# Kernel tuning notes

Measured on AMD Instinct MI355X. Metric: run time of the kernel, lower is better.

## Reference

```python
import jax, jax.numpy as jnp
import numpy as np

K = 2
BN_EPS = 1e-5


def setup_inputs() -> dict:
    key = jax.random.key(0)
    k1, k2, k3 = jax.random.split(key, 3)
    B, C, H, W, D, O = 4, 128, 32, 32, 32, 128
    x = jax.random.normal(k1, (B, C, H, W, D), dtype=jnp.float32)
    conv_w = jax.random.normal(k2, (O, 2 * C), dtype=jnp.float32) * 0.02  # 1x1x1 conv kernel
    conv_b = jax.random.normal(k3, (O,), dtype=jnp.float32) * 0.02
    bn_gamma = jnp.ones((O,), dtype=jnp.float32)
    bn_beta = jnp.zeros((O,), dtype=jnp.float32)
    return {"x": x, "conv_w": conv_w, "conv_b": conv_b,
            "bn_gamma": bn_gamma, "bn_beta": bn_beta}


def _axis_running_max(x, x_j, axis, dim):
    # torch.cat([x[..., -i:], x[..., :-i]], axis) == jnp.roll(x, i, axis)
    shifts = jnp.arange(K, dim, K)

    def step(carry, s):
        diff = x - jnp.roll(x, s, axis=axis)
        return jnp.maximum(carry, diff), None

    x_j, _ = jax.lax.scan(step, x_j, shifts)
    return x_j


def reference(x, conv_w, conv_b, bn_gamma, bn_beta):
    B, C, H, W, D = x.shape
    x_j = jnp.zeros_like(x)
    x_j = _axis_running_max(x, x_j, 2, H)
    x_j = _axis_running_max(x, x_j, 3, W)
    x_j = _axis_running_max(x, x_j, 4, D)
    x_j = jax.lax.stop_gradient(x_j)  # original detaches every x_j update

    xc = jnp.concatenate([x, x_j], axis=1)  # [B, 2C, H, W, D]
    # 1x1x1 Conv3d == per-voxel channel GEMM
    y = jnp.einsum('bchwd,oc->bohwd', xc, conv_w) + conv_b[None, :, None, None, None]

    # BatchNorm3d, training mode (batch statistics over B,H,W,D)
    mean = y.mean(axis=(0, 2, 3, 4), keepdims=True)
    var = ((y - mean) ** 2).mean(axis=(0, 2, 3, 4), keepdims=True)
    yn = (y - mean) * jax.lax.rsqrt(var + BN_EPS)
    yn = yn * bn_gamma[None, :, None, None, None] + bn_beta[None, :, None, None, None]

    # torch nn.GELU default is exact erf form
    return jax.nn.gelu(yn, approximate=False)
```

## Files before the change

### kernel.cpp

```cpp
#include <hip/hip_runtime.h>
#include <hip/hip_bf16.h>

#define BB 4
#define CCH 128
#define C2 256
#define OO 128
#define NVOX 32768
#define NTOT (BB*NVOX)
#define NGB 1024

typedef __attribute__((ext_vector_type(4))) float f32x4;
typedef __attribute__((ext_vector_type(8))) short s16x8;
typedef __attribute__((ext_vector_type(4))) unsigned int u32x4;
typedef __attribute__((ext_vector_type(2))) unsigned int u32x2;
typedef unsigned int u32;
typedef unsigned short u16;

#define SWZ(r) ((((r)>>3) ^ (r)) & 7)

__device__ __forceinline__ float bf2f(short s){
  union { u32 i; float f; } cv; cv.i = ((u32)(u16)s) << 16; return cv.f;
}
__device__ __forceinline__ short f2bf(float f){
  union { __hip_bfloat16 h; short s; } cv; cv.h = __float2bfloat16(f); return cv.s;
}
__device__ __forceinline__ u32 pack2(float a, float b){
  return ((u32)(u16)f2bf(a)) | (((u32)(u16)f2bf(b)) << 16);
}
__device__ __forceinline__ float ulo(u32 r){
  union { u32 i; float f; } cv; cv.i = r << 16; return cv.f;
}
__device__ __forceinline__ float uhi(u32 r){
  union { u32 i; float f; } cv; cv.i = r & 0xffff0000u; return cv.f;
}

__global__ __launch_bounds__(256) void k_convw(const float* __restrict__ w, short* __restrict__ wb){
  int i = blockIdx.x*256 + threadIdx.x;
  wb[i] = f2bf(w[i]);
}


__device__ __forceinline__ int swz3(int h, int w, int bin){
  int s1 = ((w>>1) ^ h) & 3;
  int s2 = ((w>>3) ^ (h>>2)) & 3;
  return (h<<11) + ((w ^ s2)<<6) + ((bin & 15) | (((((bin>>4)) ^ s1) & 3) << 4));
}

__global__ __launch_bounds__(512, 4) void k_xj(const float* __restrict__ x, short* __restrict__ xc){
  __shared__ __align__(16) u32 xs[16384];
  __shared__ __align__(16) u32 tw[2048];
  __shared__ __align__(16) u32 th[2048];
  int t = threadIdx.x;
  u32 bc = blockIdx.x;
  const float* __restrict__ src = x + (size_t)bc*NVOX;

  #pragma unroll
  for(int j=0;j<16;j++){
    int e0 = (t + 512*j)*4;
    f32x4 v = *(const f32x4*)(src + e0);
    int h = e0>>10, w = (e0>>5)&31, bin = (e0&31)*2;
    u32* dst = (u32*)((char*)xs + swz3(h,w,bin));
    dst[0] = pack2(v[0], v[1]);
    dst[1] = pack2(v[2], v[3]);
  }
  __syncthreads();

  {
    int dq = t & 7, aa = (t >> 3) & 31;
    float m1[2][4], m2[2][4];
    #pragma unroll
    for(int p=0;p<2;p++)
      #pragma unroll
      for(int k=0;k<4;k++){ m1[p][k]=1e30f; m2[p][k]=1e30f; }
    if(t < 256){
      int h = aa;
      #pragma unroll
      for(int w=0;w<32;w++){
        int p = w & 1;
        u32x2 g = *(const u32x2*)((const char*)xs + swz3(h,w,dq*8));
        #pragma unroll
        for(int q=0;q<2;q++){
          float a = ulo(g[q]), b = uhi(g[q]);
          m2[p][2*q]   = fminf(m2[p][2*q],   fmaxf(m1[p][2*q],   a)); m1[p][2*q]   = fminf(m1[p][2*q],   a);
          m2[p][2*q+1] = fminf(m2[p][2*q+1], fmaxf(m1[p][2*q+1], b)); m1[p][2*q+1] = fminf(m1[p][2*q+1], b);
        }
      }
      #pragma unroll
      for(int p=0;p<2;p++){
        u32 o0 = pack2(m1[p][0], m2[p][0]), o1 = pack2(m1[p][1], m2[p][1]);
        u32 o2 = pack2(m1[p][2], m2[p][2]), o3 = pack2(m1[p][3], m2[p][3]);
        *(u32x4*)&tw[h*64 + p*32 + dq*4] = (u32x4){o0,o1,o2,o3};
      }
    } else {
      int w = aa;
      #pragma unroll
      for(int h=0;h<32;h++){
        int p = h & 1;
        u32x2 g = *(const u32x2*)((const char*)xs + swz3(h,w,dq*8));
        #pragma unroll
        for(int q=0;q<2;q++){
          float a = ulo(g[q]), b = uhi(g[q]);
          m2[p][2*q]   = fminf(m2[p][2*q],   fmaxf(m1[p][2*q],   a)); m1[p][2*q]   = fminf(m1[p][2*q],   a);
          m2[p][2*q+1] = fminf(m2[p][2*q+1], fmaxf(m1[p][2*q+1], b)); m1[p][2*q+1] = fminf(m1[p][2*q+1], b);
        }
      }
      #pragma unroll
      for(int p=0;p<2;p++){
        u32 o0 = pack2(m1[p][0], m2[p][0]), o1 = pack2(m1[p][1], m2[p][1]);
        u32 o2 = pack2(m1[p][2], m2[p][2]), o3 = pack2(m1[p][3], m2[p][3]);
        *(u32x4*)&th[p*1024 + w*32 + ((dq ^ (w&7))*4)] = (u32x4){o0,o1,o2,o3};
      }
    }
  }
  __syncthreads();

  short* __restrict__ px = xc + ((size_t)((bc>>7)*C2 + (bc&127)))*NVOX;
  short* __restrict__ pj = px + (size_t)CCH*NVOX;
  #pragma unroll
  for(int j=0;j<2;j++){
    int l = t + 512*j;
    int h = l>>5, w = l&31;
    u32x4 xr[4];
    #pragma unroll
    for(int g=0;g<4;g++)
      xr[g] = *(const u32x4*)((const char*)xs + swz3(h,w,g<<4));
    float xv[32];
    #pragma unroll
    for(int g=0;g<4;g++)
      #pragma unroll
      for(int q=0;q<4;q++){
        xv[g*8+2*q]   = ulo(xr[g][q]);
        xv[g*8+2*q+1] = uhi(xr[g][q]);
      }
    float m1d[2] = {1e30f,1e30f}, m2d[2] = {1e30f,1e30f};
    #pragma unroll
    for(int q=0;q<16;q++){
      m2d[0] = fminf(m2d[0], fmaxf(m1d[0], xv[2*q]));   m1d[0] = fminf(m1d[0], xv[2*q]);
      m2d[1] = fminf(m2d[1], fmaxf(m1d[1], xv[2*q+1])); m1d[1] = fminf(m1d[1], xv[2*q+1]);
    }
    const u32* twr = &tw[h*64 + (w&1)*32];
    int thbase = (h&1)*1024 + w*32, ws7 = w&7;
    u32 xjp[16];
    #pragma unroll
    for(int q=0;q<8;q++){
      u32x4 wv = *(const u32x4*)(twr + q*4);
      u32x4 hv = *(const u32x4*)(&th[thbase + ((q ^ ws7)*4)]);
      float o4[4];
      #pragma unroll
      for(int i=0;i<4;i++){
        int d = q*4 + i, p = d & 1;
        float xvv = xv[d];
        float meD = (xvv == m1d[p]) ? m2d[p] : m1d[p];
        float w1 = ulo(wv[i]);
        float meW = (xvv == w1) ? uhi(wv[i]) : w1;
        float h1 = ulo(hv[i]);
        float meH = (xvv == h1) ? uhi(hv[i]) : h1;
        float m = fminf(meD, fminf(meW, meH));
        o4[i] = fmaxf(0.0f, xvv - m);
      }
      xjp[q*2]   = pack2(o4[0], o4[1]);
      xjp[q*2+1] = pack2(o4[2], o4[3]);
    }
    #pragma unroll
    for(int g=0;g<4;g++){
      *(u32x4*)(px + (size_t)l*32 + g*8) = xr[g];
      *(u32x4*)(pj + (size_t)l*32 + g*8) = (u32x4){xjp[g*4],xjp[g*4+1],xjp[g*4+2],xjp[g*4+3]};
    }
  }
}

__global__ __launch_bounds__(256) void k_gemm(const short* __restrict__ xc, const short* __restrict__ wb,
                                              short* __restrict__ y, float* __restrict__ part){
  __shared__ __align__(16) char lds[32768];
  u32 blk = blockIdx.x;
  u32 vblk = blk & 255, b = blk >> 8;
  u32 vbase = vblk * 128;
  const short* __restrict__ xb = xc + (size_t)b*C2*NVOX + vbase;
  int t = threadIdx.x;
  int wave = t >> 6, lane = t & 63;
  int wr = wave >> 1, wc = wave & 1;
  int l15 = lane & 15, l4 = lane >> 4;
  f32x4 acc[4][4];
  #pragma unroll
  for(int mt=0;mt<4;mt++)
    #pragma unroll
    for(int nt=0;nt<4;nt++) acc[mt][nt] = (f32x4){0.f,0.f,0.f,0.f};

  int v0  = (t & 15) * 8;
  int cb2 = 2 * (t >> 4);

  #pragma unroll
  for(int kc=0;kc<2;kc++){
    s16x8 ra[4], rb[4];
    #pragma unroll
    for(int q=0;q<4;q++){
      const short* src = xb + (size_t)(kc*128 + cb2 + 32*q)*NVOX + v0;
      ra[q] = *(const s16x8*)(src);
      rb[q] = *(const s16x8*)(src + NVOX);
    }
    __syncthreads();
    #pragma unroll
    for(int q=0;q<4;q++){
      int c = cb2 + 32*q;
      #pragma unroll
      for(int e=0;e<8;e++){
        int v = v0 + e;
        u32 pr = ((u32)(u16)ra[q][e]) | (((u32)(u16)rb[q][e]) << 16);
        *(u32*)(lds + v*256 + ((((c>>3) ^ SWZ(v))<<4) | ((c&7)<<1))) = pr;
      }
    }
    __syncthreads();
    #pragma unroll
    for(int ks=0;ks<4;ks++){
      int kk = ks*32 + l4*8;
      s16x8 afrag[4], bfrag[4];
      #pragma unroll
      for(int nt=0;nt<4;nt++){
        int vloc = wc*64 + nt*16 + l15;
        bfrag[nt] = *(const s16x8*)(lds + vloc*256 + (((kk>>3) ^ SWZ(vloc))<<4));
      }
      #pragma unroll
      for(int mt=0;mt<4;mt++){
        int o = wr*64 + mt*16 + l15;
        afrag[mt] = *(const s16x8*)(wb + o*C2 + kc*128 + kk);
      }
      #pragma unroll
      for(int mt=0;mt<4;mt++)
        #pragma unroll
        for(int nt=0;nt<4;nt++)
          acc[mt][nt] = __builtin_amdgcn_mfma_f32_16x16x32_bf16(afrag[mt], bfrag[nt], acc[mt][nt], 0,0,0);
    }
  }

  __syncthreads();
  #pragma unroll
  for(int mt=0;mt<4;mt++){
    #pragma unroll
    for(int nt=0;nt<4;nt++){
      int vcol = wc*64 + nt*16 + l15;
      #pragma unroll
      for(int r=0;r<4;r++){
        int o = wr*64 + mt*16 + l4*4 + r;
        *(short*)(lds + o*256 + ((((vcol>>3) ^ SWZ(o))<<4) | ((vcol&7)<<1))) = f2bf(acc[mt][nt][r]);
      }
    }
  }
  __syncthreads();
  short* __restrict__ yb = y + (size_t)b*OO*NVOX + vbase;
  #pragma unroll
  for(int q=0;q<8;q++){
    int p = t + q*256;
    int o = p >> 4, vs = (p & 15) * 8;
    s16x8 val = *(const s16x8*)(lds + o*256 + ((((vs>>3) ^ SWZ(o))<<4)));
    *(s16x8*)(yb + (size_t)o*NVOX + vs) = val;
  }

  {
    int o = t >> 1, vh = t & 1;
    float sm = 0.f, ss = 0.f;
    #pragma unroll
    for(int k=0;k<8;k++){
      int vs = vh*64 + k*8;
      s16x8 val = *(const s16x8*)(lds + o*256 + ((((vs>>3) ^ SWZ(o))<<4)));
      #pragma unroll
      for(int e=0;e<8;e++){ float f = bf2f(val[e]); sm += f; ss += f*f; }
    }
    sm += __shfl_xor(sm, 1);
    ss += __shfl_xor(ss, 1);
    if(vh == 0){
      float* pp = part + ((size_t)blk*OO + o)*2;
      pp[0] = sm; pp[1] = ss;
    }
  }
}

__global__ __launch_bounds__(256) void k_statsf(const float* __restrict__ part, float* __restrict__ stats){
  int o = blockIdx.x, t = threadIdx.x;
  float sm = 0.f, ss = 0.f;
  #pragma unroll
  for(int k=0;k<4;k++){
    int blk = t + k*256;
    const float* pp = part + ((size_t)blk*OO + o)*2;
    sm += pp[0]; ss += pp[1];
  }
  __shared__ float rs[256], rss[256];
  rs[t] = sm; rss[t] = ss;
  __syncthreads();
  for(int k=128;k>0;k>>=1){
    if(t<k){ rs[t]+=rs[t+k]; rss[t]+=rss[t+k]; }
    __syncthreads();
  }
  if(t==0){
    float inv = 1.0f/(float)NTOT;
    float mean = rs[0]*inv;
    float var = rss[0]*inv - mean*mean;
    stats[2*o]   = mean;
    stats[2*o+1] = rsqrtf(var + 1e-5f);
  }
}

__global__ __launch_bounds__(256) void k_bngelu(const short* __restrict__ y, const float* __restrict__ stats,
                                                const float* __restrict__ gamma, const float* __restrict__ beta,
                                                float* __restrict__ out){
  size_t base = ((size_t)blockIdx.x*256 + threadIdx.x)*8;
  int o = (int)((base >> 15) & 127);
  float mean = stats[2*o], rstd = stats[2*o+1];
  float g  = gamma[o]*rstd;
  float be = beta[o] - mean*g;
  s16x8 u = *(const s16x8*)(y + base);
  f32x4 r0, r1;
  #pragma unroll
  for(int e=0;e<8;e++){
    float yn = bf2f(u[e])*g + be;
    float ge = 0.5f*yn*(1.0f + erff(yn*0.70710678118654752f));
    if(e<4) r0[e] = ge; else r1[e-4] = ge;
  }
  *(f32x4*)(out + base)     = r0;
  *(f32x4*)(out + base + 4) = r1;
}

extern "C" void kernel_launch(void* const* d_in, const int* in_sizes, int n_in,
                              void* d_out, int out_size, void* d_ws, size_t ws_size,
                              hipStream_t stream) {
  (void)in_sizes; (void)n_in; (void)out_size; (void)ws_size;
  const float* x     = (const float*)d_in[0];
  const float* cw    = (const float*)d_in[1];
  const float* gamma = (const float*)d_in[3];
  const float* beta  = (const float*)d_in[4];
  float* out = (float*)d_out;

  char* ws = (char*)d_ws;
  short* wb    = (short*)ws;
  short* y     = (short*)(ws + 65536);
  float* stats = (float*)(ws + 65536 + (size_t)BB*OO*NVOX*2);
  float* part  = stats + 256;
  short* xcbuf = (short*)d_out;

  k_convw <<<dim3((OO*C2)/256),     dim3(256), 0, stream>>>(cw, wb);
  k_xj    <<<dim3(BB*CCH),         dim3(512), 0, stream>>>(x, xcbuf);
  k_gemm  <<<dim3(BB*(NVOX/128)),  dim3(256), 0, stream>>>(xcbuf, wb, y, part);
  k_statsf<<<dim3(OO),             dim3(256), 0, stream>>>(part, stats);
  k_bngelu<<<dim3((NTOT*OO)/2048), dim3(256), 0, stream>>>(y, stats, gamma, beta, out);
}
```

Measured before the change: 98.80 us.

## Drop LDS staging of x slab in prep kernel; read axis minima from global

The prep kernel no longer stages the full 32x32x32 bf16 slab in a 64KB shared buffer. The W and H axis two-smallest reductions now read x directly from global memory, with each thread handling one (h,d) or (w,d) line. The per-row D pass reloads its row from global. This frees most of the shared memory so more blocks can be resident per CU. In exchange each x element is read from global about three times, relying on cache hits, and the strided W/H reads are scalar loads.

```diff
diff --git a/kernel.cpp b/kernel.cpp
--- a/kernel.cpp
+++ b/kernel.cpp
@@ -7,12 +7,10 @@
 #define OO 128
 #define NVOX 32768
 #define NTOT (BB*NVOX)
-#define NGB 1024
 
 typedef __attribute__((ext_vector_type(4))) float f32x4;
 typedef __attribute__((ext_vector_type(8))) short s16x8;
 typedef __attribute__((ext_vector_type(4))) unsigned int u32x4;
-typedef __attribute__((ext_vector_type(2))) unsigned int u32x2;
 typedef unsigned int u32;
 typedef unsigned short u16;
 
@@ -33,21 +31,14 @@
 __device__ __forceinline__ float uhi(u32 r){
   union { u32 i; float f; } cv; cv.i = r & 0xffff0000u; return cv.f;
 }
+__device__ __forceinline__ float bfr(float f){ return bf2f(f2bf(f)); }
 
 __global__ __launch_bounds__(256) void k_convw(const float* __restrict__ w, short* __restrict__ wb){
   int i = blockIdx.x*256 + threadIdx.x;
   wb[i] = f2bf(w[i]);
 }
 
-
-__device__ __forceinline__ int swz3(int h, int w, int bin){
-  int s1 = ((w>>1) ^ h) & 3;
-  int s2 = ((w>>3) ^ (h>>2)) & 3;
-  return (h<<11) + ((w ^ s2)<<6) + ((bin & 15) | (((((bin>>4)) ^ s1) & 3) << 4));
-}
-
-__global__ __launch_bounds__(512, 4) void k_xj(const float* __restrict__ x, short* __restrict__ xc){
-  __shared__ __align__(16) u32 xs[16384];
+__global__ __launch_bounds__(512) void k_prep(const float* __restrict__ x, short* __restrict__ xc){
   __shared__ __align__(16) u32 tw[2048];
   __shared__ __align__(16) u32 th[2048];
   int t = threadIdx.x;
@@ -55,62 +46,33 @@
   const float* __restrict__ src = x + (size_t)bc*NVOX;
 
   #pragma unroll
-  for(int j=0;j<16;j++){
-    int e0 = (t + 512*j)*4;
-    f32x4 v = *(const f32x4*)(src + e0);
-    int h = e0>>10, w = (e0>>5)&31, bin = (e0&31)*2;
-    u32* dst = (u32*)((char*)xs + swz3(h,w,bin));
-    dst[0] = pack2(v[0], v[1]);
-    dst[1] = pack2(v[2], v[3]);
-  }
-  __syncthreads();
-
-  {
-    int dq = t & 7, aa = (t >> 3) & 31;
-    float m1[2][4], m2[2][4];
-    #pragma unroll
-    for(int p=0;p<2;p++)
-      #pragma unroll
-      for(int k=0;k<4;k++){ m1[p][k]=1e30f; m2[p][k]=1e30f; }
-    if(t < 256){
-      int h = aa;
-      #pragma unroll
-      for(int w=0;w<32;w++){
-        int p = w & 1;
-        u32x2 g = *(const u32x2*)((const char*)xs + swz3(h,w,dq*8));
-        #pragma unroll
-        for(int q=0;q<2;q++){
-          float a = ulo(g[q]), b = uhi(g[q]);
-          m2[p][2*q]   = fminf(m2[p][2*q],   fmaxf(m1[p][2*q],   a)); m1[p][2*q]   = fminf(m1[p][2*q],   a);
-          m2[p][2*q+1] = fminf(m2[p][2*q+1], fmaxf(m1[p][2*q+1], b)); m1[p][2*q+1] = fminf(m1[p][2*q+1], b);
-        }
-      }
-      #pragma unroll
-      for(int p=0;p<2;p++){
-        u32 o0 = pack2(m1[p][0], m2[p][0]), o1 = pack2(m1[p][1], m2[p][1]);
-        u32 o2 = pack2(m1[p][2], m2[p][2]), o3 = pack2(m1[p][3], m2[p][3]);
-        *(u32x4*)&tw[h*64 + p*32 + dq*4] = (u32x4){o0,o1,o2,o3};
-      }
-    } else {
-      int w = aa;
-      #pragma unroll
-      for(int h=0;h<32;h++){
-        int p = h & 1;
-        u32x2 g = *(const u32x2*)((const char*)xs + swz3(h,w,dq*8));
-        #pragma unroll
-        for(int q=0;q<2;q++){
-          float a = ulo(g[q]), b = uhi(g[q]);
-          m2[p][2*q]   = fminf(m2[p][2*q],   fmaxf(m1[p][2*q],   a)); m1[p][2*q]   = fminf(m1[p][2*q],   a);
-          m2[p][2*q+1] = fminf(m2[p][2*q+1], fmaxf(m1[p][2*q+1], b)); m1[p][2*q+1] = fminf(m1[p][2*q+1], b);
-        }
-      }
-      #pragma unroll
-      for(int p=0;p<2;p++){
-        u32 o0 = pack2(m1[p][0], m2[p][0]), o1 = pack2(m1[p][1], m2[p][1]);
-        u32 o2 = pack2(m1[p][2], m2[p][2]), o3 = pack2(m1[p][3], m2[p][3]);
-        *(u32x4*)&th[p*1024 + w*32 + ((dq ^ (w&7))*4)] = (u32x4){o0,o1,o2,o3};
-      }
-    }
+  for(int j=0;j<2;j++){
+    int task = t + 512*j;
+    int h = task >> 5, d = task & 31;
+    float m1[2]={1e30f,1e30f}, m2[2]={1e30f,1e30f};
+    #pragma unroll 4
+    for(int w=0;w<32;w++){
+      float v = bfr(src[h*1024 + w*32 + d]);
+      int p = w & 1;
+      m2[p] = fminf(m2[p], fmaxf(m1[p], v)); m1[p] = fminf(m1[p], v);
+    }
+    tw[h*64 + d]      = pack2(m1[0], m2[0]);
+    tw[h*64 + 32 + d] = pack2(m1[1], m2[1]);
+  }
+  #pragma unroll
+  for(int j=0;j<2;j++){
+    int task = t + 512*j;
+    int w = task >> 5, d = task & 31;
+    float m1[2]={1e30f,1e30f}, m2[2]={1e30f,1e30f};
+    #pragma unroll 4
+    for(int h=0;h<32;h++){
+      float v = bfr(src[h*1024 + w*32 + d]);
+      int p = h & 1;
+      m2[p] = fminf(m2[p], fmaxf(m1[p], v)); m1[p] = fminf(m1[p], v);
+    }
+    int slot = (d & 3) | ((((d>>2) ^ (w&7)) & 7) << 2);
+    th[w*32 + slot]        = pack2(m1[0], m2[0]);
+    th[1024 + w*32 + slot] = pack2(m1[1], m2[1]);
   }
   __syncthreads();
 
@@ -119,52 +81,49 @@
   #pragma unroll
   for(int j=0;j<2;j++){
     int l = t + 512*j;
-    int h = l>>5, w = l&31;
-    u32x4 xr[4];
-    #pragma unroll
-    for(int g=0;g<4;g++)
-      xr[g] = *(const u32x4*)((const char*)xs + swz3(h,w,g<<4));
+    int h = l >> 5, w = l & 31;
+    const float* pl = src + l*32;
+    u32 xp[16];
+    #pragma unroll
+    for(int g=0;g<8;g++){
+      f32x4 v = *(const f32x4*)(pl + g*4);
+      xp[g*2]   = pack2(v[0], v[1]);
+      xp[g*2+1] = pack2(v[2], v[3]);
+    }
     float xv[32];
     #pragma unroll
-    for(int g=0;g<4;g++)
-      #pragma unroll
-      for(int q=0;q<4;q++){
-        xv[g*8+2*q]   = ulo(xr[g][q]);
-        xv[g*8+2*q+1] = uhi(xr[g][q]);
-      }
-    float m1d[2] = {1e30f,1e30f}, m2d[2] = {1e30f,1e30f};
+    for(int g=0;g<16;g++){ xv[2*g] = ulo(xp[g]); xv[2*g+1] = uhi(xp[g]); }
+    float m1d[2]={1e30f,1e30f}, m2d[2]={1e30f,1e30f};
     #pragma unroll
     for(int q=0;q<16;q++){
       m2d[0] = fminf(m2d[0], fmaxf(m1d[0], xv[2*q]));   m1d[0] = fminf(m1d[0], xv[2*q]);
       m2d[1] = fminf(m2d[1], fmaxf(m1d[1], xv[2*q+1])); m1d[1] = fminf(m1d[1], xv[2*q+1]);
     }
     const u32* twr = &tw[h*64 + (w&1)*32];
-    int thbase = (h&1)*1024 + w*32, ws7 = w&7;
-    u32 xjp[16];
-    #pragma unroll
-    for(int q=0;q<8;q++){
-      u32x4 wv = *(const u32x4*)(twr + q*4);
-      u32x4 hv = *(const u32x4*)(&th[thbase + ((q ^ ws7)*4)]);
+    int thb = (h&1)*1024 + w*32, ws7 = w&7;
+    u32 jp[16];
+    #pragma unroll
+    for(int g=0;g<8;g++){
+      u32x4 wv = *(const u32x4*)(twr + g*4);
+      u32x4 hv = *(const u32x4*)(&th[thb + ((g ^ ws7)<<2)]);
       float o4[4];
       #pragma unroll
       for(int i=0;i<4;i++){
-        int d = q*4 + i, p = d & 1;
+        int d = g*4 + i, p = d & 1;
         float xvv = xv[d];
-        float meD = (xvv == m1d[p]) ? m2d[p] : m1d[p];
-        float w1 = ulo(wv[i]);
-        float meW = (xvv == w1) ? uhi(wv[i]) : w1;
-        float h1 = ulo(hv[i]);
-        float meH = (xvv == h1) ? uhi(hv[i]) : h1;
-        float m = fminf(meD, fminf(meW, meH));
-        o4[i] = fmaxf(0.0f, xvv - m);
-      }
-      xjp[q*2]   = pack2(o4[0], o4[1]);
-      xjp[q*2+1] = pack2(o4[2], o4[3]);
+        float mD = (xvv == m1d[p]) ? m2d[p] : m1d[p];
+        float w1 = ulo(wv[i]); float mW = (xvv == w1) ? uhi(wv[i]) : w1;
+        float h1 = ulo(hv[i]); float mH = (xvv == h1) ? uhi(hv[i]) : h1;
+        float mn = fminf(mD, fminf(mW, mH));
+        o4[i] = fmaxf(0.0f, xvv - mn);
+      }
+      jp[g*2]   = pack2(o4[0], o4[1]);
+      jp[g*2+1] = pack2(o4[2], o4[3]);
     }
     #pragma unroll
     for(int g=0;g<4;g++){
-      *(u32x4*)(px + (size_t)l*32 + g*8) = xr[g];
-      *(u32x4*)(pj + (size_t)l*32 + g*8) = (u32x4){xjp[g*4],xjp[g*4+1],xjp[g*4+2],xjp[g*4+3]};
+      *(u32x4*)(px + (size_t)l*32 + g*8) = (u32x4){xp[g*4],xp[g*4+1],xp[g*4+2],xp[g*4+3]};
+      *(u32x4*)(pj + (size_t)l*32 + g*8) = (u32x4){jp[g*4],jp[g*4+1],jp[g*4+2],jp[g*4+3]};
     }
   }
 }
@@ -337,7 +296,7 @@
   short* xcbuf = (short*)d_out;
 
   k_convw <<<dim3((OO*C2)/256),     dim3(256), 0, stream>>>(cw, wb);
-  k_xj    <<<dim3(BB*CCH),         dim3(512), 0, stream>>>(x, xcbuf);
+  k_prep  <<<dim3(BB*CCH),         dim3(512), 0, stream>>>(x, xcbuf);
   k_gemm  <<<dim3(BB*(NVOX/128)),  dim3(256), 0, stream>>>(xcbuf, wb, y, part);
   k_statsf<<<dim3(OO),             dim3(256), 0, stream>>>(part, stats);
   k_bngelu<<<dim3((NTOT*OO)/2048), dim3(256), 0, stream>>>(y, stats, gamma, beta, out);
```

Result: slower. 111.4 us (+12.7%).
